# Kernel tuning notes

Hardware: AMD Instinct MI355X
Metric: run time of the kernel (lower is better)

The kernel has to match this reference:

```python
import jax, jax.numpy as jnp
import numpy as np

BETA = 0.904837
V_TH = 1.0
SURR_K = 25.0


def _spike(v):
    # Heaviside forward; surrogate gradient irrelevant for fwd-only.
    return (v >= V_TH).astype(v.dtype)


def setup_inputs() -> dict:
    key = jax.random.key(0)
    k1, k2 = jax.random.split(key)
    B, T, H = 16, 1024, 2048
    input_current = jax.random.normal(k1, (B, T, H), dtype=jnp.float32)
    v_init = jax.random.normal(k2, (B, H), dtype=jnp.float32)
    return {"input_current": input_current, "v_init": v_init}


def reference(input_current, v_init):
    # input_current: (B, T, H), v_init: (B, H)
    def step(carry, i_t):
        v, s_prev = carry
        v = BETA * v * (1.0 - s_prev) + i_t  # hard reset via (1 - s_prev)
        s = _spike(v)
        return (v, s), (s, v)

    s0 = jnp.zeros_like(v_init)
    # scan over time axis: move T to leading dim
    (v_final, _), (spikes_t, membrane_t) = jax.lax.scan(
        step, (v_init, s0), jnp.swapaxes(input_current, 0, 1)
    )
    spikes = jnp.swapaxes(spikes_t, 0, 1)      # (B, T, H)
    membrane = jnp.swapaxes(membrane_t, 0, 1)  # (B, T, H)
    return spikes, membrane, v_final
```

## Files before the change

### kernel.cpp

```cpp
#include <hip/hip_runtime.h>


constexpr int B_ = 16;
constexpr int T_ = 1024;
constexpr int H_ = 2048;
constexpr int H2 = H_ / 2;
constexpr float BETA = 0.904837f;
constexpr int C  = 32;
constexpr int NCH = T_ / C;
constexpr int PAIRS = C / 2;

typedef __attribute__((ext_vector_type(2))) float fx2;

__device__ __forceinline__ void async_copy16(const void* g, void* s) {
    __builtin_amdgcn_global_load_lds(
        (const __attribute__((address_space(1))) void*)g,
        (__attribute__((address_space(3))) void*)s,
        16, 0, 0);
}

__global__ __launch_bounds__(64) void lif_fwd_kernel(
    const float* __restrict__ in,
    const float* __restrict__ v0,
    fx2* __restrict__ sp,
    fx2* __restrict__ mem,
    fx2* __restrict__ vf)
{
    __shared__ fx2 lds_buf[2][C * 64];

    const int lane = threadIdx.x;
    const int w    = blockIdx.x;
    const int b    = w >> 4;
    const int colb = (w & 15) * 64;

    const size_t seq_base = (size_t)b * T_ * H2 + colb;

    const int sel = lane >> 5;
    const char* stage_base = (const char*)in + seq_base * 8
                           + (size_t)sel * (H2 * 8)
                           + (size_t)(lane & 31) * 16;

    fx2* __restrict__ spp = sp  + seq_base + lane;
    fx2* __restrict__ mpp = mem + seq_base + lane;

    const int vidx = b * H2 + colb + lane;
    const fx2 vv = ((const fx2*)v0)[vidx];
    float v0r = vv[0], v1r = vv[1];
    float s0r = 0.0f, s1r = 0.0f;

#pragma unroll
    for (int p = 0; p < PAIRS; ++p)
        async_copy16(stage_base + (size_t)(2 * p) * (H2 * 8),
                     &lds_buf[0][p * 128]);

    for (int c = 0; c < NCH; ++c) {
        __syncthreads();

        if (c + 1 < NCH) {
            const char* gb = stage_base + (size_t)(c + 1) * C * (H2 * 8);
            const int nb = (c + 1) & 1;
#pragma unroll
            for (int p = 0; p < PAIRS; ++p)
                async_copy16(gb + (size_t)(2 * p) * (H2 * 8),
                             &lds_buf[nb][p * 128]);
        }

        const fx2* lbuf = lds_buf[c & 1];
        const size_t obase = (size_t)c * C * H2;
#pragma unroll
        for (int s = 0; s < C; ++s) {
            const fx2 x = lbuf[s * 64 + lane];

            v0r = BETA * v0r * (1.0f - s0r) + x[0];
            v1r = BETA * v1r * (1.0f - s1r) + x[1];
            s0r = (v0r >= 1.0f) ? 1.0f : 0.0f;
            s1r = (v1r >= 1.0f) ? 1.0f : 0.0f;

            const size_t o = obase + (size_t)s * H2;
            fx2 sv; sv[0] = s0r; sv[1] = s1r;
            fx2 mv; mv[0] = v0r; mv[1] = v1r;
            __builtin_nontemporal_store(sv, spp + o);
            __builtin_nontemporal_store(mv, mpp + o);
        }
    }

    fx2 vfv; vfv[0] = v0r; vfv[1] = v1r;
    vf[vidx] = vfv;
}

extern "C" void kernel_launch(void* const* d_in, const int* in_sizes, int n_in,
                              void* d_out, int out_size, void* d_ws, size_t ws_size,
                              hipStream_t stream) {
    const float* in = (const float*)d_in[0];
    const float* v0 = (const float*)d_in[1];

    float* out = (float*)d_out;
    const size_t n_bth = (size_t)B_ * T_ * H_;
    fx2* sp  = (fx2*)out;
    fx2* mem = (fx2*)(out + n_bth);
    fx2* vf  = (fx2*)(out + 2 * n_bth);

    const int grid = B_ * (H2 / 64);
    lif_fwd_kernel<<<grid, 64, 0, stream>>>(in, v0, sp, mem, vf);
}
```

Baseline: 358.7 us.

## Use one column per lane, a 4-deep LDS prefetch ring, and explicit vmcnt waits

Each lane now handles one float column instead of two, which doubles the grid to 512 single-wave blocks. Chunks shrink to 16 timesteps and go into a 4-buffer LDS ring with a prefetch distance of 3. The per-chunk __syncthreads is replaced by hand-counted s_waitcnt vmcnt values, so loads stay in flight across output stores. This aims at more parallel waves and deeper load/store overlap, at the cost of scalar 4-byte stores and fragile counter assumptions that depend on how the compiler emits the nontemporal stores.

```diff
diff --git a/kernel.cpp b/kernel.cpp
--- a/kernel.cpp
+++ b/kernel.cpp
@@ -1,16 +1,14 @@
 #include <hip/hip_runtime.h>
 
 
-constexpr int B_ = 16;
-constexpr int T_ = 1024;
-constexpr int H_ = 2048;
-constexpr int H2 = H_ / 2;
+constexpr int B_  = 16;
+constexpr int T_  = 1024;
+constexpr int H_  = 2048;
 constexpr float BETA = 0.904837f;
-constexpr int C  = 32;
+
+constexpr int C   = 16;
 constexpr int NCH = T_ / C;
-constexpr int PAIRS = C / 2;
-
-typedef __attribute__((ext_vector_type(2))) float fx2;
+constexpr int OPS = (C * 64) / (64 * 4);
 
 __device__ __forceinline__ void async_copy16(const void* g, void* s) {
     __builtin_amdgcn_global_load_lds(
@@ -22,70 +20,64 @@
 __global__ __launch_bounds__(64) void lif_fwd_kernel(
     const float* __restrict__ in,
     const float* __restrict__ v0,
-    fx2* __restrict__ sp,
-    fx2* __restrict__ mem,
-    fx2* __restrict__ vf)
+    float* __restrict__ sp,
+    float* __restrict__ mem,
+    float* __restrict__ vf)
 {
-    __shared__ fx2 lds_buf[2][C * 64];
+    __shared__ float lds_buf[4][C * 64];
 
     const int lane = threadIdx.x;
     const int w    = blockIdx.x;
-    const int b    = w >> 4;
-    const int colb = (w & 15) * 64;
+    const int b    = w >> 5;
+    const int col  = (w & 31) * 64;
 
-    const size_t seq_base = (size_t)b * T_ * H2 + colb;
+    const size_t seq = (size_t)b * T_ * H_ + col;
 
-    const int sel = lane >> 5;
-    const char* stage_base = (const char*)in + seq_base * 8
-                           + (size_t)sel * (H2 * 8)
-                           + (size_t)(lane & 31) * 16;
+    const char* sbase = (const char*)(in + seq)
+                      + (size_t)(lane >> 4) * (H_ * 4)
+                      + (size_t)(lane & 15) * 16;
 
-    fx2* __restrict__ spp = sp  + seq_base + lane;
-    fx2* __restrict__ mpp = mem + seq_base + lane;
+    float* __restrict__ spp = sp  + seq + lane;
+    float* __restrict__ mpp = mem + seq + lane;
 
-    const int vidx = b * H2 + colb + lane;
-    const fx2 vv = ((const fx2*)v0)[vidx];
-    float v0r = vv[0], v1r = vv[1];
-    float s0r = 0.0f, s1r = 0.0f;
+    const int vidx = b * H_ + col + lane;
+    float v = v0[vidx];
+    float s = 0.0f;
 
+    auto stage = [&](int c) {
+        const char* gb = sbase + (size_t)c * C * (H_ * 4);
 #pragma unroll
-    for (int p = 0; p < PAIRS; ++p)
-        async_copy16(stage_base + (size_t)(2 * p) * (H2 * 8),
-                     &lds_buf[0][p * 128]);
+        for (int p = 0; p < OPS; ++p)
+            async_copy16(gb + (size_t)(4 * p) * (H_ * 4),
+                         &lds_buf[c & 3][p * 256]);
+    };
+
+    stage(0); stage(1); stage(2);
+    asm volatile("s_waitcnt vmcnt(8)" ::: "memory");
 
     for (int c = 0; c < NCH; ++c) {
-        __syncthreads();
+        const float* lbuf = lds_buf[c & 3];
+        const size_t obase = (size_t)c * C * H_;
+#pragma unroll
+        for (int t = 0; t < C; ++t) {
+            const float x = lbuf[t * 64 + lane];
 
-        if (c + 1 < NCH) {
-            const char* gb = stage_base + (size_t)(c + 1) * C * (H2 * 8);
-            const int nb = (c + 1) & 1;
-#pragma unroll
-            for (int p = 0; p < PAIRS; ++p)
-                async_copy16(gb + (size_t)(2 * p) * (H2 * 8),
-                             &lds_buf[nb][p * 128]);
+            v = BETA * v * (1.0f - s) + x;
+            s = (v >= 1.0f) ? 1.0f : 0.0f;
+
+            const size_t o = obase + (size_t)t * H_;
+            __builtin_nontemporal_store(s, spp + o);
+            __builtin_nontemporal_store(v, mpp + o);
         }
 
-        const fx2* lbuf = lds_buf[c & 1];
-        const size_t obase = (size_t)c * C * H2;
-#pragma unroll
-        for (int s = 0; s < C; ++s) {
-            const fx2 x = lbuf[s * 64 + lane];
+        if (c + 3 < NCH) stage(c + 3);
 
-            v0r = BETA * v0r * (1.0f - s0r) + x[0];
-            v1r = BETA * v1r * (1.0f - s1r) + x[1];
-            s0r = (v0r >= 1.0f) ? 1.0f : 0.0f;
-            s1r = (v1r >= 1.0f) ? 1.0f : 0.0f;
-
-            const size_t o = obase + (size_t)s * H2;
-            fx2 sv; sv[0] = s0r; sv[1] = s1r;
-            fx2 mv; mv[0] = v0r; mv[1] = v1r;
-            __builtin_nontemporal_store(sv, spp + o);
-            __builtin_nontemporal_store(mv, mpp + o);
-        }
+        if (c + 3 < NCH)       asm volatile("s_waitcnt vmcnt(40)" ::: "memory");
+        else if (c + 2 < NCH)  asm volatile("s_waitcnt vmcnt(36)" ::: "memory");
+        else if (c + 1 < NCH)  asm volatile("s_waitcnt vmcnt(32)" ::: "memory");
     }
 
-    fx2 vfv; vfv[0] = v0r; vfv[1] = v1r;
-    vf[vidx] = vfv;
+    vf[vidx] = v;
 }
 
 extern "C" void kernel_launch(void* const* d_in, const int* in_sizes, int n_in,
@@ -96,10 +88,10 @@
 
     float* out = (float*)d_out;
     const size_t n_bth = (size_t)B_ * T_ * H_;
-    fx2* sp  = (fx2*)out;
-    fx2* mem = (fx2*)(out + n_bth);
-    fx2* vf  = (fx2*)(out + 2 * n_bth);
+    float* sp  = out;
+    float* mem = out + n_bth;
+    float* vf  = out + 2 * n_bth;
 
-    const int grid = B_ * (H2 / 64);
+    const int grid = B_ * (H_ / 64);
     lif_fwd_kernel<<<grid, 64, 0, stream>>>(in, v0, sp, mem, vf);
 }
```

After: 365.7 us. Within noise of the previous version (+1.9%).
